# Optimization experiments

Measured on AMD Instinct MI355X. Metric: run time of the kernel, lower is better.

Reference implementation:

```python
import jax, jax.numpy as jnp
import numpy as np

N, M, C_IN, T, V = 64, 2, 3, 300, 25
C_ENC, C_DEC, K = 64, 64, 3
INTER = C_ENC // 4  # coff_embedding = 4 in 2s-AGCN unit_gcn
EPS_BN = 1e-5


def _bn(x, gamma, beta):
    # nn.BatchNorm2d in training mode: biased batch stats over (N, H, W), channel axis=1
    mean = x.mean(axis=(0, 2, 3), keepdims=True)
    var = x.var(axis=(0, 2, 3), keepdims=True)
    return gamma[None, :, None, None] * (x - mean) * jax.lax.rsqrt(var + EPS_BN) + beta[None, :, None, None]


def _unit_gcn(x, A, PA, wa, ba, wb, bb, wd, bd, gamma, beta, down_fn):
    # x: (N,C,T,V); A,PA: (K,V,V); wa/wb: (K,inter,C); wd: (K,Cout,C)  (1x1 convs)
    n, c, t, v = x.shape
    inter = wa.shape[1]
    Ahat = A + PA
    fa = jnp.einsum('nctv,kic->nkitv', x, wa) + ba[None, :, :, None, None]
    fb = jnp.einsum('nctv,kic->nkitv', x, wb) + bb[None, :, :, None, None]
    # torch: matmul((N,V,inter*T),(N,inter*T,V)) / (inter*T), softmax over dim -2 (rows)
    att = jnp.einsum('nkitv,nkitw->nkvw', fa, fb) / (inter * t)
    att = jax.nn.softmax(att, axis=-2) + Ahat[None]
    z = jnp.einsum('nctv,nkvw->nkctw', x, att)           # (N,K,C,T,V)
    y = jnp.einsum('nkctw,koc->notw', z, wd) + bd.sum(0)[None, :, None, None]
    y = _bn(y, gamma, beta)
    y = y + down_fn(x)
    return jax.nn.relu(y)


def _forward(x, A, integration_param, ram_gamma, ram_beta,
             enc_PA, enc_wa, enc_ba, enc_wb, enc_bb, enc_wd, enc_bd, enc_gamma, enc_beta,
             enc_dw, enc_db, enc_dgamma, enc_dbeta,
             dec_PA, dec_wa, dec_ba, dec_wb, dec_bb, dec_wd, dec_bd, dec_gamma, dec_beta):
    xa = x[:, 0]  # (N,C,T,V) person a
    xb = x[:, 1]  # (N,C,T,V) person b

    # --- geometric component ---
    g = jnp.einsum('nctv,nctw->nctvw', jnp.exp(xa), jnp.exp(-xb))  # (N,C,T,V,V)
    g = jnp.log(g + 1e-5) ** 2
    RAM_g = jnp.exp((-1.0 / 3.0) * g.sum(axis=1))                  # (N,T,V,V)

    # --- relative attention component ---
    enc_down = lambda h: _bn(jnp.einsum('nctv,oc->notv', h, enc_dw) + enc_db[None, :, None, None],
                             enc_dgamma, enc_dbeta)
    ident = lambda h: h  # decoder has in==out channels -> identity residual
    p1 = _unit_gcn(xa, A, enc_PA, enc_wa, enc_ba, enc_wb, enc_bb, enc_wd, enc_bd, enc_gamma, enc_beta, enc_down)
    p2 = _unit_gcn(xb, A, enc_PA, enc_wa, enc_ba, enc_wb, enc_bb, enc_wd, enc_bd, enc_gamma, enc_beta, enc_down)
    p1 = _unit_gcn(p1, A, dec_PA, dec_wa, dec_ba, dec_wb, dec_bb, dec_wd, dec_bd, dec_gamma, dec_beta, ident)
    p2 = _unit_gcn(p2, A, dec_PA, dec_wa, dec_ba, dec_wb, dec_bb, dec_wd, dec_bd, dec_gamma, dec_beta, ident)
    RAM_r = jnp.einsum('nctv,nctw->ntvw', p1, p2)                  # (N,T,V,V)
    RAM_r = _bn(RAM_r, ram_gamma, ram_beta)                        # BN over T channels
    RAM_r = (jnp.tanh(RAM_r) + 1.0) / 2.0                          # scaledTanh

    pct = (jnp.tanh(integration_param) + 1.0) / 2.0                # scalar gate
    RAM = pct * RAM_r + (1.0 - pct) * RAM_g

    # abnormal mask: variance over joints (dim=3, unbiased), summed over channels
    ab = jnp.var(xb, axis=3, ddof=1).sum(axis=1)                   # (N,T)
    ab = jnp.where(ab < 1e-4, 0.0, 1.0)
    RAM = RAM * ab[:, :, None, None]

    # normalizeRAM
    RAM = jnp.where(RAM < 0.5, 0.0, RAM)
    da = RAM.sum(axis=2)                                           # (N,T,W)
    db = RAM.sum(axis=3)                                           # (N,T,V)
    norm = jnp.einsum('ntv,ntw->ntvw', db, da)
    RAM = RAM * jax.lax.rsqrt(norm + 1e-5)
    return RAM


def setup_inputs() -> dict:
    key = jax.random.key(0)
    ks = jax.random.split(key, 12)
    f32 = jnp.float32
    rn = lambda k, s, sc=0.1: jax.random.normal(k, s, dtype=f32) * sc
    inp = {}
    inp['x'] = jax.random.normal(ks[0], (N, M, C_IN, T, V), dtype=f32)
    inp['A'] = jax.random.uniform(ks[1], (K, V, V), dtype=f32)
    inp['integration_param'] = jnp.zeros((1,), f32)
    inp['ram_gamma'] = jnp.ones((T,), f32)
    inp['ram_beta'] = jnp.zeros((T,), f32)
    inp['enc_PA'] = rn(ks[2], (K, V, V), 1e-3)
    inp['enc_wa'] = rn(ks[3], (K, INTER, C_IN)); inp['enc_ba'] = jnp.zeros((K, INTER), f32)
    inp['enc_wb'] = rn(ks[4], (K, INTER, C_IN)); inp['enc_bb'] = jnp.zeros((K, INTER), f32)
    inp['enc_wd'] = rn(ks[5], (K, C_ENC, C_IN)); inp['enc_bd'] = jnp.zeros((K, C_ENC), f32)
    inp['enc_gamma'] = jnp.ones((C_ENC,), f32); inp['enc_beta'] = jnp.zeros((C_ENC,), f32)
    inp['enc_dw'] = rn(ks[6], (C_ENC, C_IN)); inp['enc_db'] = jnp.zeros((C_ENC,), f32)
    inp['enc_dgamma'] = jnp.ones((C_ENC,), f32); inp['enc_dbeta'] = jnp.zeros((C_ENC,), f32)
    inp['dec_PA'] = rn(ks[7], (K, V, V), 1e-3)
    inp['dec_wa'] = rn(ks[8], (K, INTER, C_ENC)); inp['dec_ba'] = jnp.zeros((K, INTER), f32)
    inp['dec_wb'] = rn(ks[9], (K, INTER, C_ENC)); inp['dec_bb'] = jnp.zeros((K, INTER), f32)
    inp['dec_wd'] = rn(ks[10], (K, C_DEC, C_ENC)); inp['dec_bd'] = jnp.zeros((K, C_DEC), f32)
    inp['dec_gamma'] = jnp.ones((C_DEC,), f32); inp['dec_beta'] = jnp.zeros((C_DEC,), f32)
    return inp


def reference(x, A, integration_param, ram_gamma, ram_beta,
              enc_PA, enc_wa, enc_ba, enc_wb, enc_bb, enc_wd, enc_bd, enc_gamma, enc_beta,
              enc_dw, enc_db, enc_dgamma, enc_dbeta,
              dec_PA, dec_wa, dec_ba, dec_wb, dec_bb, dec_wd, dec_bd, dec_gamma, dec_beta):
    return _forward(x, A, integration_param, ram_gamma, ram_beta,
                    enc_PA, enc_wa, enc_ba, enc_wb, enc_bb, enc_wd, enc_bd, enc_gamma, enc_beta,
                    enc_dw, enc_db, enc_dgamma, enc_dbeta,
                    dec_PA, dec_wa, dec_ba, dec_wb, dec_bb, dec_wd, dec_bd, dec_gamma, dec_beta)
```

## Files before the change

### kernel.cpp

```cpp
#include <hip/hip_runtime.h>
#include <math.h>

#define N_     64
#define Mn     2
#define Tn     300
#define Vn     25
#define Kk     3
#define CIN    3
#define CE     64
#define INTER_ 16
#define TV     7500
#define VV     625
#define ESEG   5
#define DSEG   15
#define EYB    12

typedef float f4 __attribute__((ext_vector_type(4)));
typedef float f2 __attribute__((ext_vector_type(2)));

#define OFF_ATTP  0L
#define OFF_PART  0L
#define OFF_ATTEP 1200000L
#define OFF_ATTDP 1468800L
#define OFF_COV   1776000L
#define OFF_PCT   1780320L
#define OFF_YC    1781088L
#define OFF_TST   1781344L
#define OFF_DWDT  1781944L
#define OFF_WABT  1794232L
#define WS_REQ    1800376L

#define AEP_BR 134400
#define ADP_BR 153600

__global__ __launch_bounds__(640)
void att_kernel(const float* __restrict__ x,
                const float* __restrict__ wa, const float* __restrict__ ba,
                const float* __restrict__ wb, const float* __restrict__ bb,
                float* __restrict__ att_partial)
{
    int b = blockIdx.x;
    int s = b % ESEG;
    int k = (b / ESEG) % Kk;
    int n = (b / (ESEG * Kk)) % N_;
    int br = b / (ESEG * Kk * N_);
    const float* xp = x + (long)br * (CIN * TV) + (long)n * (Mn * CIN * TV);

    __shared__ float xs[CIN][Vn];
    __shared__ float fa_s[INTER_][Vn];
    __shared__ float fb_s[INTER_][Vn];

    int tid = threadIdx.x;
    float acc = 0.f;
    const int TSEG = Tn / ESEG;
    int t0 = s * TSEG;
    for (int t = t0; t < t0 + TSEG; ++t) {
        __syncthreads();
        for (int idx = tid; idx < CIN * Vn; idx += 640) {
            int c = idx / Vn, v = idx % Vn;
            xs[c][v] = xp[(long)c * TV + t * Vn + v];
        }
        __syncthreads();
        for (int idx = tid; idx < 2 * INTER_ * Vn; idx += 640) {
            int j = idx;
            const float* w; const float* bias; float (*dst)[Vn];
            if (j < INTER_ * Vn) { w = wa; bias = ba; dst = fa_s; }
            else { j -= INTER_ * Vn; w = wb; bias = bb; dst = fb_s; }
            int i = j / Vn, v = j % Vn;
            float sum = bias[k * INTER_ + i];
            const float* wr = w + (k * INTER_ + i) * CIN;
            #pragma unroll
            for (int c = 0; c < CIN; ++c) sum += wr[c] * xs[c][v];
            dst[i][v] = sum;
        }
        __syncthreads();
        if (tid < VV) {
            int v = tid / Vn, w = tid % Vn;
            float a = 0.f;
            #pragma unroll
            for (int i = 0; i < INTER_; ++i) a += fa_s[i][v] * fb_s[i][w];
            acc += a;
        }
    }
    if (tid < VV)
        att_partial[(((long)((br * N_ + n) * Kk + k)) * ESEG + s) * VV + tid] = acc;
}

template<int SEGS, int PADW>
__global__ __launch_bounds__(256)
void softmax_kernel(const float* __restrict__ att_partial,
                    const float* __restrict__ A, const float* __restrict__ PA,
                    float* __restrict__ attP)
{
    int b = blockIdx.x;
    int k = b % Kk;
    __shared__ float as[VV];
    int tid = threadIdx.x;
    for (int idx = tid; idx < VV; idx += 256) {
        float s = 0.f;
        for (int seg = 0; seg < SEGS; ++seg)
            s += att_partial[((long)b * SEGS + seg) * VV + idx];
        as[idx] = s * (1.0f / (INTER_ * Tn));
    }
    __syncthreads();
    if (tid < Vn) {
        int w = tid;
        float m = -1e30f;
        #pragma unroll
        for (int v = 0; v < Vn; ++v) m = fmaxf(m, as[v * Vn + w]);
        float e[Vn];
        float den = 0.f;
        #pragma unroll
        for (int v = 0; v < Vn; ++v) { e[v] = expf(as[v * Vn + w] - m); den += e[v]; }
        float inv = 1.f / den;
        #pragma unroll
        for (int v = 0; v < Vn; ++v)
            attP[((long)b * Vn + v) * PADW + w] =
                e[v] * inv + A[k * VV + v * Vn + w] + PA[k * VV + v * Vn + w];
    } else if (tid < PADW) {
        #pragma unroll
        for (int v = 0; v < Vn; ++v)
            attP[((long)b * Vn + v) * PADW + tid] = 0.f;
    }
}

__global__ __launch_bounds__(256)
void xcov_kernel(const float* __restrict__ x, double* __restrict__ part)
{
    int br = blockIdx.x / 120, g = blockIdx.x % 120;
    const float* xbase = x + (long)br * (CIN * TV);
    double a[9];
    #pragma unroll
    for (int q = 0; q < 9; ++q) a[q] = 0.0;
    for (long idx = (long)g * 256 + threadIdx.x; idx < (long)N_ * TV;
         idx += 120L * 256) {
        int n = (int)(idx / TV);
        int j = (int)(idx % TV);
        const float* xp = xbase + (long)n * (Mn * CIN * TV) + j;
        float x0 = xp[0], x1 = xp[TV], x2 = xp[2 * TV];
        a[0] += x0; a[1] += x1; a[2] += x2;
        a[3] += (double)x0 * x0; a[4] += (double)x0 * x1; a[5] += (double)x0 * x2;
        a[6] += (double)x1 * x1; a[7] += (double)x1 * x2; a[8] += (double)x2 * x2;
    }
    __shared__ double red[256];
    int tid = threadIdx.x;
    for (int q = 0; q < 9; ++q) {
        red[tid] = a[q];
        __syncthreads();
        for (int off = 128; off > 0; off >>= 1) {
            if (tid < off) red[tid] += red[tid + off];
            __syncthreads();
        }
        if (tid == 0) part[(long)blockIdx.x * 9 + q] = red[0];
        __syncthreads();
    }
}

__global__ __launch_bounds__(256)
void ey_stat_kernel(const float* __restrict__ x, const float* __restrict__ attEpB,
                    const float* __restrict__ ewd, float* __restrict__ part)
{
    __shared__ float attE_s[Kk][Vn][Vn];
    __shared__ float ewd_s[Kk * CE * CIN];
    __shared__ float xs[CIN][Vn];
    __shared__ float ez[Kk * CIN * Vn];
    __shared__ float ys[CE][Vn];
    int b = blockIdx.x, tb = b % EYB, n = (b / EYB) % N_, br = b / (EYB * N_);
    const float* attEp = attEpB + (long)br * AEP_BR;
    const float* xb = x + (long)br * (CIN * TV);
    int tid = threadIdx.x;
    for (int i = tid; i < Kk * VV; i += 256) {
        int k = i / 625, r = i - k * 625, v = r / 25, w = r - (r / 25) * 25;
        ((float*)attE_s)[i] = attEp[(long)n * 2100 + (k * 25 + v) * 28 + w];
    }
    for (int i = tid; i < Kk * CE * CIN; i += 256) ewd_s[i] = ewd[i];
    float s1 = 0.f, s2 = 0.f;
    for (int t = tb * 25; t < tb * 25 + 25; ++t) {
        const float* xp = xb + (long)n * (Mn * CIN * TV) + t * Vn;
        __syncthreads();
        for (int i = tid; i < CIN * Vn; i += 256) { int c = i / Vn, v = i % Vn; xs[c][v] = xp[c * TV + v]; }
        __syncthreads();
        for (int i = tid; i < Kk * CIN * Vn; i += 256) {
            int w = i % Vn, c = (i / Vn) % CIN, k = i / (Vn * CIN);
            float s = 0.f;
            #pragma unroll
            for (int v = 0; v < Vn; ++v) s += xs[c][v] * attE_s[k][v][w];
            ez[i] = s;
        }
        __syncthreads();
        for (int i = tid; i < CE * Vn; i += 256) {
            int w = i % Vn, o = i / Vn;
            float y = 0.f;
            #pragma unroll
            for (int k = 0; k < Kk; ++k)
                #pragma unroll
                for (int c = 0; c < CIN; ++c)
                    y += ewd_s[(k * CE + o) * CIN + c] * ez[(k * CIN + c) * Vn + w];
            ys[o][w] = y;
        }
        __syncthreads();
        if (tid < CE) {
            #pragma unroll
            for (int w = 0; w < Vn; ++w) { float y = ys[tid][w]; s1 += y; s2 += y * y; }
        }
    }
    if (tid < CE) { part[(long)b * 128 + tid * 2] = s1; part[(long)b * 128 + tid * 2 + 1] = s2; }
}

__global__ __launch_bounds__(64)
void enc_fin_kernel(const float* __restrict__ partB,
                    const double* __restrict__ covpB,
                    const float* __restrict__ eg, const float* __restrict__ ebt,
                    const float* __restrict__ edw, const float* __restrict__ edb,
                    const float* __restrict__ edg, const float* __restrict__ edbt,
                    float* __restrict__ pcTB)
{
    int br = blockIdx.x;
    const float* part = partB + (long)br * (N_ * EYB * 128);
    const double* covp = covpB + (long)br * (120 * 9);
    float* pcT = pcTB + br * 384;
    int o = threadIdx.x;
    __shared__ double tot[9];
    if (o < 9) { double s = 0; for (int g = 0; g < 120; ++g) s += covp[(long)g * 9 + o]; tot[o] = s; }
    double s1 = 0, s2 = 0;
    for (int b = 0; b < N_ * EYB; ++b) { s1 += part[(long)b * 128 + o * 2]; s2 += part[(long)b * 128 + o * 2 + 1]; }
    __syncthreads();
    double cnt = (double)N_ * Tn * Vn;
    double mean = s1 / cnt, var = s2 / cnt - mean * mean;
    double ersig = 1.0 / sqrt(var + 1e-5);
    double alpha = (double)eg[o] * ersig;
    double inv = 1.0 / cnt;
    double mu0 = tot[0] * inv, mu1 = tot[1] * inv, mu2 = tot[2] * inv;
    double c00 = tot[3] * inv - mu0 * mu0, c01 = tot[4] * inv - mu0 * mu1, c02 = tot[5] * inv - mu0 * mu2;
    double c11 = tot[6] * inv - mu1 * mu1, c12 = tot[7] * inv - mu1 * mu2, c22 = tot[8] * inv - mu2 * mu2;
    double w0 = edw[o * CIN + 0], w1 = edw[o * CIN + 1], w2 = edw[o * CIN + 2];
    double dmean = w0 * mu0 + w1 * mu1 + w2 * mu2 + (double)edb[o];
    double dvar = w0 * w0 * c00 + w1 * w1 * c11 + w2 * w2 * c22
                + 2.0 * (w0 * w1 * c01 + w0 * w2 * c02 + w1 * w2 * c12);
    double drsig = 1.0 / sqrt(dvar + 1e-5);
    double dga = (double)edg[o] * drsig;
    pcT[0 * 64 + o] = (float)alpha;
    pcT[1 * 64 + o] = (float)((double)ebt[o] - (double)eg[o] * mean * ersig
                              + dga * ((double)edb[o] - dmean) + (double)edbt[o]);
    pcT[2 * 64 + o] = (float)(dga * w0);
    pcT[3 * 64 + o] = (float)(dga * w1);
    pcT[4 * 64 + o] = (float)(dga * w2);
    pcT[5 * 64 + o] = 0.f;
}

__global__ __launch_bounds__(256)
void tr_dwd_kernel(const float* __restrict__ dwd, float* __restrict__ outp)
{
    int i = blockIdx.x * 256 + threadIdx.x;
    if (i < Kk * CE * CE) {
        int k = i / (CE * CE), r = i % (CE * CE);
        int o = r >> 6, c = r & 63;
        outp[((long)k * CE + c) * CE + o] = dwd[i];
    }
}

__global__ __launch_bounds__(256)
void tr_wab_kernel(const float* __restrict__ dwa, const float* __restrict__ dwb,
                   float* __restrict__ outp)
{
    int i = blockIdx.x * 256 + threadIdx.x;
    if (i < CE * 96) {
        int c = i / 96, j = i % 96;
        float v = (j < 48) ? dwa[j * CE + c] : dwb[(j - 48) * CE + c];
        outp[i] = v;
    }
}

__device__ __forceinline__ void penc_tile(int tid, int NT, const float* xp,
    const float (*attE_s)[Vn][Vn], const float* ewd_s, const float (*pc_s)[6],
    float (*xs)[Vn], float* ez, float (*ps)[26])
{
    __syncthreads();
    for (int i = tid; i < CIN * Vn; i += NT) { int c = i / Vn, v = i % Vn; xs[c][v] = xp[c * TV + v]; }
    __syncthreads();
    for (int i = tid; i < Kk * CIN * Vn; i += NT) {
        int w = i % Vn, c = (i / Vn) % CIN, k = i / (Vn * CIN);
        float s = 0.f;
        #pragma unroll
        for (int v = 0; v < Vn; ++v) s += xs[c][v] * attE_s[k][v][w];
        ez[i] = s;
    }
    __syncthreads();
    for (int i = tid; i < CE * Vn; i += NT) {
        int w = i % Vn, o = i / Vn;
        float y = 0.f;
        #pragma unroll
        for (int k = 0; k < Kk; ++k)
            #pragma unroll
            for (int c = 0; c < CIN; ++c)
                y += ewd_s[(k * CE + o) * CIN + c] * ez[(k * CIN + c) * Vn + w];
        float val = pc_s[o][0] * y + pc_s[o][1]
                  + pc_s[o][2] * xs[0][w] + pc_s[o][3] * xs[1][w] + pc_s[o][4] * xs[2][w];
        ps[o][w] = fmaxf(val, 0.f);
    }
    for (int i = tid; i < CE; i += NT) ps[i][25] = 0.f;
    __syncthreads();
}

__global__ __launch_bounds__(512)
void datt_kernel(const float* __restrict__ x, const float* __restrict__ attEpB,
                 const float* __restrict__ ewd, const float* __restrict__ pcTB,
                 const float* __restrict__ wabTg,
                 const float* __restrict__ dba, const float* __restrict__ dbb,
                 float* __restrict__ attp)
{
    __shared__ float attE_s[Kk][Vn][Vn];
    __shared__ float ewd_s[Kk * CE * CIN];
    __shared__ float pc_s[CE][6];
    __shared__ float bias_s[96];
    __shared__ float xs[CIN][Vn];
    __shared__ float ez[Kk * CIN * Vn];
    __shared__ __align__(16) float ps[CE][26];
    __shared__ __align__(16) float fab[96][26];
    int b = blockIdx.x, s = b % DSEG, n = (b / DSEG) % N_, br = b / (DSEG * N_);
    const float* attEp = attEpB + (long)br * AEP_BR;
    const float* pcT = pcTB + br * 384;
    const float* xb = x + (long)br * (CIN * TV);
    int tid = threadIdx.x;
    for (int i = tid; i < Kk * VV; i += 512) {
        int k = i / 625, r = i - k * 625, v = r / 25, w = r - (r / 25) * 25;
        ((float*)attE_s)[i] = attEp[(long)n * 2100 + (k * 25 + v) * 28 + w];
    }
    for (int i = tid; i < Kk * CE * CIN; i += 512) ewd_s[i] = ewd[i];
    for (int i = tid; i < CE * 6; i += 512) pc_s[i & 63][i >> 6] = pcT[i];
    for (int i = tid; i < 96; i += 512) bias_s[i] = (i < 48) ? dba[i] : dbb[i - 48];

    int sk = tid / 169, sr = tid % 169;
    int sv0 = (sr / 13) * 2, sw0 = (sr % 13) * 2;
    float acc00 = 0.f, acc01 = 0.f, acc10 = 0.f, acc11 = 0.f;
    int fj0 = (tid / 13) * 4, fv0 = (tid % 13) * 2;

    const int TS = Tn / DSEG;
    for (int t = s * TS; t < s * TS + TS; ++t) {
        const float* xp = xb + (long)n * (Mn * CIN * TV) + t * Vn;
        penc_tile(tid, 512, xp, attE_s, ewd_s, pc_s, xs, ez, ps);
        if (tid < 312) {
            float ft[4][2] = {{0.f,0.f},{0.f,0.f},{0.f,0.f},{0.f,0.f}};
            const float* wg = wabTg + fj0;
            #pragma unroll 8
            for (int c = 0; c < 64; ++c) {
                f4 wv = *(const f4*)&wg[c * 96];
                f2 pv = *(const f2*)&ps[c][fv0];
                #pragma unroll
                for (int j = 0; j < 4; ++j) {
                    ft[j][0] += wv[j] * pv[0];
                    ft[j][1] += wv[j] * pv[1];
                }
            }
            #pragma unroll
            for (int j = 0; j < 4; ++j) {
                f2 r = { ft[j][0] + bias_s[fj0 + j], ft[j][1] + bias_s[fj0 + j] };
                *(f2*)&fab[fj0 + j][fv0] = r;
            }
        }
        __syncthreads();
        if (tid < 507) {
            #pragma unroll
            for (int i = 0; i < INTER_; ++i) {
                f2 a = *(const f2*)&fab[sk * INTER_ + i][sv0];
                f2 bb2 = *(const f2*)&fab[48 + sk * INTER_ + i][sw0];
                acc00 += a[0] * bb2[0]; acc01 += a[0] * bb2[1];
                acc10 += a[1] * bb2[0]; acc11 += a[1] * bb2[1];
            }
        }
    }
    if (tid < 507) {
        long ob = (((long)((br * N_ + n) * Kk + sk)) * DSEG + s) * VV;
        attp[ob + sv0 * 25 + sw0] = acc00;
        if (sw0 + 1 < 25)                 attp[ob + sv0 * 25 + sw0 + 1] = acc01;
        if (sv0 + 1 < 25)                 attp[ob + (sv0 + 1) * 25 + sw0] = acc10;
        if (sv0 + 1 < 25 && sw0 + 1 < 25) attp[ob + (sv0 + 1) * 25 + sw0 + 1] = acc11;
    }
}

template<int TTC>
__global__ __launch_bounds__(128)
void decy0_kernel(const float* __restrict__ x,
                  const float* __restrict__ attEp,
                  const float* __restrict__ attDp,
                  const float* __restrict__ ewd,
                  const float* __restrict__ pcTg,
                  const float* __restrict__ dwdTg,
                  float* __restrict__ outp)
{
    constexpr int TBc = Tn / TTC;
    __shared__ __align__(16) float psT[25][68];
    __shared__ __align__(16) float dz_s[64][36];
    __shared__ __align__(16) float attD_s[Kk][25][32];
    __shared__ __align__(16) float ewdT_s[9][64];
    __shared__ __align__(16) float ez_s[9][28];
    __shared__ float xs[3][25];

    int b = blockIdx.x;
    int br = b / (N_ * TBc);
    int rem = b - br * (N_ * TBc);
    int n = rem / TBc, tb = rem - (rem / TBc) * TBc;
    int tid = threadIdx.x;
    int tq = tid >> 3, tw8 = tid & 7;
    int q0 = tq * 4, w0 = tw8 * 4;

    for (int i = tid; i < 576; i += 128) {
        int kc = i >> 6, o = i & 63;
        int k = kc / 3, c = kc - k * 3;
        ewdT_s[kc][o] = ewd[(k * 64 + o) * 3 + c];
    }
    for (int i = tid; i < 600; i += 128) {
        int r = i * 4;
        *(f4*)&((float*)attD_s)[r] = *(const f4*)&attDp[(long)br * ADP_BR + n * 2400 + r];
    }

    float s1_[4] = {0.f,0.f,0.f,0.f}, s2_[4] = {0.f,0.f,0.f,0.f};

    for (int tt = 0; tt < TTC; ++tt) {
        int t = tb * TTC + tt;
        __syncthreads();
        for (int i = tid; i < 75; i += 128) {
            int c = i / 25, v = i - (i / 25) * 25;
            xs[c][v] = x[(long)br * (CIN * TV) + (long)n * (Mn * CIN * TV)
                         + c * TV + t * 25 + v];
        }
        __syncthreads();
        if (tid < 72) {
            int kc = tid >> 3, wg = tid & 7;
            if (wg < 7) {
                int k = kc / 3, c = kc - k * 3;
                const float* aE = attEp + (long)br * AEP_BR + n * 2100 + k * 700;
                float e0 = 0.f, e1 = 0.f, e2 = 0.f, e3 = 0.f;
                #pragma unroll
                for (int v = 0; v < 25; ++v) {
                    f4 ae = *(const f4*)&aE[v * 28 + wg * 4];
                    float xv = xs[c][v];
                    e0 += xv * ae[0]; e1 += xv * ae[1];
                    e2 += xv * ae[2]; e3 += xv * ae[3];
                }
                f4 r = { e0, e1, e2, e3 };
                *(f4*)&ez_s[kc][wg * 4] = r;
            }
        }
        __syncthreads();
        for (int g = tid; g < 400; g += 128) {
            int og = (g & 15) << 2, w = g >> 4;
            float y0 = 0.f, y1 = 0.f, y2 = 0.f, y3 = 0.f;
            #pragma unroll
            for (int kc = 0; kc < 9; ++kc) {
                f4 wt = *(const f4*)&ewdT_s[kc][og];
                float ev = ez_s[kc][w];
                y0 += wt[0] * ev; y1 += wt[1] * ev;
                y2 += wt[2] * ev; y3 += wt[3] * ev;
            }
            const float* pcb = pcTg + br * 384;
            f4 al = *(const f4*)&pcb[0 * 64 + og];
            f4 be = *(const f4*)&pcb[1 * 64 + og];
            f4 d0 = *(const f4*)&pcb[2 * 64 + og];
            f4 d1 = *(const f4*)&pcb[3 * 64 + og];
            f4 d2 = *(const f4*)&pcb[4 * 64 + og];
            float x0 = xs[0][w], x1 = xs[1][w], x2 = xs[2][w];
            f4 r;
            r[0] = fmaxf(al[0] * y0 + be[0] + d0[0] * x0 + d1[0] * x1 + d2[0] * x2, 0.f);
            r[1] = fmaxf(al[1] * y1 + be[1] + d0[1] * x0 + d1[1] * x1 + d2[1] * x2, 0.f);
            r[2] = fmaxf(al[2] * y2 + be[2] + d0[2] * x0 + d1[2] * x1 + d2[2] * x2, 0.f);
            r[3] = fmaxf(al[3] * y3 + be[3] + d0[3] * x0 + d1[3] * x1 + d2[3] * x2, 0.f);
            *(f4*)&psT[w][og] = r;
        }
        float acc[4][4];
        #pragma unroll
        for (int j = 0; j < 4; ++j)
            #pragma unroll
            for (int m = 0; m < 4; ++m) acc[j][m] = 0.f;
        for (int k = 0; k < Kk; ++k) {
            __syncthreads();
            {
                float dzt[4][4];
                #pragma unroll
                for (int j = 0; j < 4; ++j)
                    #pragma unroll
                    for (int m = 0; m < 4; ++m) dzt[j][m] = 0.f;
                for (int v = 0; v < 25; ++v) {
                    f4 pa = *(const f4*)&psT[v][q0];
                    f4 ad = *(const f4*)&attD_s[k][v][w0];
                    #pragma unroll
                    for (int j = 0; j < 4; ++j)
                        #pragma unroll
                        for (int m = 0; m < 4; ++m) dzt[j][m] += pa[j] * ad[m];
                }
                #pragma unroll
                for (int j = 0; j < 4; ++j) {
                    f4 wv = { dzt[j][0], dzt[j][1], dzt[j][2], dzt[j][3] };
                    *(f4*)&dz_s[q0 + j][w0] = wv;
                }
            }
            __syncthreads();
            const float* wgp = dwdTg + k * 4096 + q0;
            #pragma unroll 8
            for (int c = 0; c < 64; ++c) {
                f4 wv = *(const f4*)&wgp[c * 64];
                f4 zv = *(const f4*)&dz_s[c][w0];
                #pragma unroll
                for (int j = 0; j < 4; ++j)
                    #pragma unroll
                    for (int m = 0; m < 4; ++m) acc[j][m] += wv[j] * zv[m];
            }
        }
        #pragma unroll
        for (int m = 0; m < 4; ++m) if (w0 + m < 25)
            #pragma unroll
            for (int j = 0; j < 4; ++j) {
                float a = acc[j][m]; s1_[j] += a; s2_[j] += a * a;
            }
    }
    float* red = (float*)dz_s;
    #pragma unroll
    for (int pass = 0; pass < 2; ++pass) {
        __syncthreads();
        #pragma unroll
        for (int j = 0; j < 4; ++j)
            red[(q0 + j) * 8 + tw8] = pass ? s2_[j] : s1_[j];
        __syncthreads();
        if (tid < 64) {
            float a = 0.f;
            #pragma unroll
            for (int q = 0; q < 8; ++q) a += red[tid * 8 + q];
            long pb = (((long)br * N_ + n) * TBc + tb) * 128;
            outp[pb + tid * 2 + pass] = a;
        }
    }
}

template<int TTC>
__global__ __launch_bounds__(256)
void decy1_kernel(const float* __restrict__ x,
                  const float* __restrict__ attEp,
                  const float* __restrict__ attDp,
                  const float* __restrict__ ewd,
                  const float* __restrict__ pcTg,
                  const float* __restrict__ ycb,
                  const float* __restrict__ dwdTg,
                  float* __restrict__ outp)
{
    constexpr int TBc = Tn / TTC;
    __shared__ __align__(16) float psT[2][25][68];
    __shared__ __align__(16) float dz_s[2][64][36];
    __shared__ __align__(16) float attD_s[2][Kk][25][32];
    __shared__ __align__(16) float ewdT_s[9][64];
    __shared__ __align__(16) float ez_s[2][9][28];
    __shared__ float xs[2][3][25];

    int b = blockIdx.x, tb = b % TBc, n = b / TBc;
    int tid = threadIdx.x;
    int u = tid >> 7, tl = tid & 127;
    int tq = tl >> 3, tw8 = tl & 7;
    int q0 = tq * 4, w0 = tw8 * 4;

    for (int i = tid; i < 576; i += 256) {
        int kc = i >> 6, o = i & 63;
        int k = kc / 3, c = kc - k * 3;
        ewdT_s[kc][o] = ewd[(k * 64 + o) * 3 + c];
    }
    for (int i = tid; i < 1200; i += 256) {
        int u2 = i / 600, r = (i - u2 * 600) * 4;
        *(f4*)&((float*)attD_s)[u2 * 2400 + r] =
            *(const f4*)&attDp[(long)u2 * ADP_BR + n * 2400 + r];
    }

    for (int tt = 0; tt < TTC; ++tt) {
        int t = tb * TTC + tt;
        __syncthreads();
        for (int i = tid; i < 150; i += 256) {
            int uu = i / 75, r = i - uu * 75, c = r / 25, v = r - (r / 25) * 25;
            xs[uu][c][v] = x[(((long)n * 2 + uu) * 3 + c) * TV + t * 25 + v];
        }
        __syncthreads();
        if (tid < 144) {
            int u2 = tid >= 72; int gg = tid - u2 * 72;
            int kc = gg >> 3, wg = gg & 7;
            if (wg < 7) {
                int k = kc / 3, c = kc - k * 3;
                const float* aE = attEp + u2 * AEP_BR + n * 2100 + k * 700;
                float e0 = 0.f, e1 = 0.f, e2 = 0.f, e3 = 0.f;
                #pragma unroll
                for (int v = 0; v < 25; ++v) {
                    f4 ae = *(const f4*)&aE[v * 28 + wg * 4];
                    float xv = xs[u2][c][v];
                    e0 += xv * ae[0]; e1 += xv * ae[1];
                    e2 += xv * ae[2]; e3 += xv * ae[3];
                }
                f4 r = { e0, e1, e2, e3 };
                *(f4*)&ez_s[u2][kc][wg * 4] = r;
            }
        }
        __syncthreads();
        for (int g = tid; g < 800; g += 256) {
            int u2 = g >= 400; int gg = g - u2 * 400;
            int og = (gg & 15) << 2, w = gg >> 4;
            float y0 = 0.f, y1 = 0.f, y2 = 0.f, y3 = 0.f;
            #pragma unroll
            for (int kc = 0; kc < 9; ++kc) {
                f4 wt = *(const f4*)&ewdT_s[kc][og];
                float ev = ez_s[u2][kc][w];
                y0 += wt[0] * ev; y1 += wt[1] * ev;
                y2 += wt[2] * ev; y3 += wt[3] * ev;
            }
            const float* pcb = pcTg + u2 * 384;
            f4 al = *(const f4*)&pcb[0 * 64 + og];
            f4 be = *(const f4*)&pcb[1 * 64 + og];
            f4 d0 = *(const f4*)&pcb[2 * 64 + og];
            f4 d1 = *(const f4*)&pcb[3 * 64 + og];
            f4 d2 = *(const f4*)&pcb[4 * 64 + og];
            float x0 = xs[u2][0][w], x1 = xs[u2][1][w], x2 = xs[u2][2][w];
            f4 r;
            r[0] = fmaxf(al[0] * y0 + be[0] + d0[0] * x0 + d1[0] * x1 + d2[0] * x2, 0.f);
            r[1] = fmaxf(al[1] * y1 + be[1] + d0[1] * x0 + d1[1] * x1 + d2[1] * x2, 0.f);
            r[2] = fmaxf(al[2] * y2 + be[2] + d0[2] * x0 + d1[2] * x1 + d2[2] * x2, 0.f);
            r[3] = fmaxf(al[3] * y3 + be[3] + d0[3] * x0 + d1[3] * x1 + d2[3] * x2, 0.f);
            *(f4*)&psT[u2][w][og] = r;
        }
        float acc[4][4];
        #pragma unroll
        for (int j = 0; j < 4; ++j)
            #pragma unroll
            for (int m = 0; m < 4; ++m) acc[j][m] = 0.f;
        for (int k = 0; k < Kk; ++k) {
            __syncthreads();
            {
                float dzt[4][4];
                #pragma unroll
                for (int j = 0; j < 4; ++j)
                    #pragma unroll
                    for (int m = 0; m < 4; ++m) dzt[j][m] = 0.f;
                for (int v = 0; v < 25; ++v) {
                    f4 pa = *(const f4*)&psT[u][v][q0];
                    f4 ad = *(const f4*)&attD_s[u][k][v][w0];
                    #pragma unroll
                    for (int j = 0; j < 4; ++j)
                        #pragma unroll
                        for (int m = 0; m < 4; ++m) dzt[j][m] += pa[j] * ad[m];
                }
                #pragma unroll
                for (int j = 0; j < 4; ++j) {
                    f4 wv = { dzt[j][0], dzt[j][1], dzt[j][2], dzt[j][3] };
                    *(f4*)&dz_s[u][q0 + j][w0] = wv;
                }
            }
            __syncthreads();
            const float* wgp = dwdTg + k * 4096 + q0;
            #pragma unroll 8
            for (int c = 0; c < 64; ++c) {
                f4 wv = *(const f4*)&wgp[c * 64];
                f4 zv = *(const f4*)&dz_s[u][c][w0];
                #pragma unroll
                for (int j = 0; j < 4; ++j)
                    #pragma unroll
                    for (int m = 0; m < 4; ++m) acc[j][m] += wv[j] * zv[m];
            }
        }
        {
            const float* ycu = ycb + u * 128;
            #pragma unroll
            for (int m = 0; m < 4; ++m) {
                int w = w0 + m;
                if (w < 25) {
                    #pragma unroll
                    for (int j = 0; j < 4; ++j) {
                        float pd = ycu[(q0 + j) * 2] * acc[j][m]
                                 + ycu[(q0 + j) * 2 + 1] + psT[u][w][q0 + j];
                        psT[u][w][q0 + j] = fmaxf(pd, 0.f);
                    }
                }
            }
        }
        __syncthreads();
        if (tid < 169) {
            int tv = tid / 13, tw2 = tid % 13;
            int v0 = tv * 2, ww0 = tw2 * 2;
            float r00 = 0.f, r01 = 0.f, r10 = 0.f, r11 = 0.f;
            for (int c = 0; c < 64; c += 4) {
                f4 a0 = *(const f4*)&psT[0][v0][c];
                f4 a1 = *(const f4*)&psT[0][v0 + 1][c];
                f4 b0 = *(const f4*)&psT[1][ww0][c];
                f4 b1 = *(const f4*)&psT[1][ww0 + 1][c];
                #pragma unroll
                for (int q = 0; q < 4; ++q) {
                    r00 += a0[q] * b0[q]; r01 += a0[q] * b1[q];
                    r10 += a1[q] * b0[q]; r11 += a1[q] * b1[q];
                }
            }
            long ob = ((long)n * Tn + t) * VV;
            outp[ob + v0 * 25 + ww0] = r00;
            if (ww0 + 1 < 25)                outp[ob + v0 * 25 + ww0 + 1] = r01;
            if (v0 + 1 < 25)                 outp[ob + (v0 + 1) * 25 + ww0] = r10;
            if (v0 + 1 < 25 && ww0 + 1 < 25) outp[ob + (v0 + 1) * 25 + ww0 + 1] = r11;
        }
    }
}

__global__ __launch_bounds__(64)
void dec_fin_kernel(const float* __restrict__ partB, int nparts,
                    const float* __restrict__ dg, const float* __restrict__ dbt,
                    float* __restrict__ ycB)
{
    int br = blockIdx.x;
    const float* part = partB + (long)br * nparts * 128;
    float* yc = ycB + br * 128;
    int o = threadIdx.x;
    double s1 = 0, s2 = 0;
    for (int b = 0; b < nparts; ++b) { s1 += part[(long)b * 128 + o * 2]; s2 += part[(long)b * 128 + o * 2 + 1]; }
    double cnt = (double)N_ * Tn * Vn;
    double mean = s1 / cnt, var = s2 / cnt - mean * mean;
    double rsig = 1.0 / sqrt(var + 1e-5);
    double a = (double)dg[o] * rsig;
    yc[o * 2 + 0] = (float)a;
    yc[o * 2 + 1] = (float)((double)dbt[o] - a * mean);
}

__global__ __launch_bounds__(256)
void rrbn_kernel(const float* __restrict__ rr, float* __restrict__ tstats)
{
    int t = blockIdx.x;
    double s = 0.0, s2 = 0.0;
    for (int idx = threadIdx.x; idx < N_ * VV; idx += 256) {
        int n = idx / VV, j = idx % VV;
        float v = rr[((long)n * Tn + t) * VV + j];
        s += v; s2 += (double)v * v;
    }
    __shared__ double rs[256], rs2[256];
    int tid = threadIdx.x;
    rs[tid] = s; rs2[tid] = s2;
    __syncthreads();
    for (int off = 128; off > 0; off >>= 1) {
        if (tid < off) { rs[tid] += rs[tid + off]; rs2[tid] += rs2[tid + off]; }
        __syncthreads();
    }
    if (tid == 0) {
        double cnt = (double)N_ * VV;
        double mean = rs[0] / cnt;
        double var = rs2[0] / cnt - mean * mean;
        tstats[t * 2 + 0] = (float)mean;
        tstats[t * 2 + 1] = (float)(1.0 / sqrt(var + 1e-5));
    }
}

__global__ __launch_bounds__(128)
void final_kernel(const float* __restrict__ tstats,
                  const float* __restrict__ x, const float* __restrict__ iparam,
                  const float* __restrict__ tgamma, const float* __restrict__ tbeta,
                  float* out)
{
    int b = blockIdx.x;
    int t = b % Tn, n = b / Tn;
    __shared__ float xa_s[CIN][Vn], xb_s[CIN][Vn];
    __shared__ float ram_s[VV];
    __shared__ float da_s[Vn], db_s[Vn];
    __shared__ float varc[CIN];
    __shared__ float abf;
    int tid = threadIdx.x;

    for (int idx = tid; idx < 2 * CIN * Vn; idx += 128) {
        int half = idx / (CIN * Vn);
        int r = idx % (CIN * Vn);
        int c = r / Vn, v = r % Vn;
        float val = x[(((long)n * Mn + half) * CIN + c) * TV + t * Vn + v];
        if (half == 0) xa_s[c][v] = val; else xb_s[c][v] = val;
    }
    __syncthreads();
    if (tid < CIN) {
        float s = 0.f, s2 = 0.f;
        #pragma unroll
        for (int v = 0; v < Vn; ++v) { float q = xb_s[tid][v]; s += q; s2 += q * q; }
        float mean = s / Vn;
        varc[tid] = (s2 - Vn * mean * mean) / (Vn - 1);
    }
    __syncthreads();
    if (tid == 0) {
        float absum = varc[0] + varc[1] + varc[2];
        abf = (absum < 1e-4f) ? 0.f : 1.f;
    }
    float pct = 0.5f * (tanhf(iparam[0]) + 1.f);
    float mt = tstats[t * 2], rt = tstats[t * 2 + 1];
    float gt = tgamma[t], bt = tbeta[t];
    __syncthreads();

    for (int idx = tid; idx < VV; idx += 128) {
        int v = idx / Vn, w = idx % Vn;
        float rrv = out[(long)b * VV + idx];
        float rbn = gt * (rrv - mt) * rt + bt;
        float ramr = 0.5f * (tanhf(rbn) + 1.f);
        float gsum = 0.f;
        #pragma unroll
        for (int c = 0; c < CIN; ++c) {
            float d = expf(xa_s[c][v]) * expf(-xb_s[c][w]);
            float l = logf(d + 1e-5f);
            gsum += l * l;
        }
        float ramg = expf(-(1.f / 3.f) * gsum);
        float ram = pct * ramr + (1.f - pct) * ramg;
        ram *= abf;
        if (ram < 0.5f) ram = 0.f;
        ram_s[idx] = ram;
    }
    __syncthreads();
    if (tid < Vn) {
        float s = 0.f;
        #pragma unroll
        for (int v = 0; v < Vn; ++v) s += ram_s[v * Vn + tid];
        da_s[tid] = s;
    } else if (tid >= 64 && tid < 64 + Vn) {
        int v = tid - 64;
        float s = 0.f;
        #pragma unroll
        for (int w = 0; w < Vn; ++w) s += ram_s[v * Vn + w];
        db_s[v] = s;
    }
    __syncthreads();
    for (int idx = tid; idx < VV; idx += 128) {
        int v = idx / Vn, w = idx % Vn;
        float ram = ram_s[idx];
        out[(long)b * VV + idx] = ram * rsqrtf(db_s[v] * da_s[w] + 1e-5f);
    }
}

extern "C" void kernel_launch(void* const* d_in, const int* in_sizes, int n_in,
                              void* d_out, int out_size, void* d_ws, size_t ws_size,
                              hipStream_t stream)
{
    const float* x    = (const float*)d_in[0];
    const float* A    = (const float*)d_in[1];
    const float* ip   = (const float*)d_in[2];
    const float* rg   = (const float*)d_in[3];
    const float* rbta = (const float*)d_in[4];
    const float* ePA  = (const float*)d_in[5];
    const float* ewa  = (const float*)d_in[6];
    const float* eba  = (const float*)d_in[7];
    const float* ewb  = (const float*)d_in[8];
    const float* ebb  = (const float*)d_in[9];
    const float* ewd  = (const float*)d_in[10];
    const float* ebd  = (const float*)d_in[11];  (void)ebd;
    const float* eg   = (const float*)d_in[12];
    const float* ebt  = (const float*)d_in[13];
    const float* edw  = (const float*)d_in[14];
    const float* edb  = (const float*)d_in[15];
    const float* edg  = (const float*)d_in[16];
    const float* edbt = (const float*)d_in[17];
    const float* dPA  = (const float*)d_in[18];
    const float* dwa  = (const float*)d_in[19];
    const float* dba  = (const float*)d_in[20];
    const float* dwb  = (const float*)d_in[21];
    const float* dbb  = (const float*)d_in[22];
    const float* dwd  = (const float*)d_in[23];
    const float* dbd  = (const float*)d_in[24];  (void)dbd;
    const float* dg   = (const float*)d_in[25];
    const float* dbt  = (const float*)d_in[26];

    if (ws_size < (size_t)WS_REQ * sizeof(float)) return;

    float* ws    = (float*)d_ws;
    float* attp  = ws + OFF_ATTP;
    float* part  = ws + OFF_PART;
    float* attEp = ws + OFF_ATTEP;
    float* attDp = ws + OFF_ATTDP;
    double* covp = (double*)(ws + OFF_COV);
    float* pcT   = ws + OFF_PCT;
    float* yc    = ws + OFF_YC;
    float* tst   = ws + OFF_TST;
    float* dwdTg = ws + OFF_DWDT;
    float* wabTg = ws + OFF_WABT;
    float* outf  = (float*)d_out;

    tr_dwd_kernel<<<(Kk * CE * CE + 255) / 256, 256, 0, stream>>>(dwd, dwdTg);
    tr_wab_kernel<<<(CE * 96 + 255) / 256, 256, 0, stream>>>(dwa, dwb, wabTg);

    att_kernel<<<2 * N_ * Kk * ESEG, 640, 0, stream>>>(
        x, ewa, eba, ewb, ebb, attp);
    softmax_kernel<ESEG, 28><<<2 * N_ * Kk, 256, 0, stream>>>(attp, A, ePA, attEp);
    xcov_kernel<<<240, 256, 0, stream>>>(x, covp);
    ey_stat_kernel<<<2 * N_ * EYB, 256, 0, stream>>>(x, attEp, ewd, part);
    enc_fin_kernel<<<2, 64, 0, stream>>>(part, covp, eg, ebt, edw, edb, edg, edbt, pcT);
    datt_kernel<<<2 * N_ * DSEG, 512, 0, stream>>>(
        x, attEp, ewd, pcT, wabTg, dba, dbb, outf);
    softmax_kernel<DSEG, 32><<<2 * N_ * Kk, 256, 0, stream>>>(outf, A, dPA, attDp);

    decy0_kernel<5><<<2 * N_ * (Tn / 5), 128, 0, stream>>>(
        x, attEp, attDp, ewd, pcT, dwdTg, part);
    dec_fin_kernel<<<2, 64, 0, stream>>>(part, N_ * (Tn / 5), dg, dbt, yc);
    decy1_kernel<3><<<N_ * (Tn / 3), 256, 0, stream>>>(
        x, attEp, attDp, ewd, pcT, yc, dwdTg, outf);

    rrbn_kernel<<<Tn, 256, 0, stream>>>(outf, tst);
    final_kernel<<<N_ * Tn, 128, 0, stream>>>(tst, x, ip, rg, rbta, outf);
}
```

Before: 3.899 ms.

## Re-tile decoder GCN kernel to process persons sequentially and stage params in LDS

The decy1 kernel now has all 256 threads work on one person at a time, each with a 4x2 output tile, instead of splitting the threads across the two persons with 4x4 tiles. This halves the dz_s shared buffer and lowers register pressure, at the cost of twice as many barrier-separated k-loop passes per time step. The pcT and yc parameter tables are copied into LDS once per block rather than read from global memory. Time steps per block drop from 3 to 2, which launches more blocks.

Result: slower. 4.426 ms (+13.5%).

```diff
diff --git a/kernel.cpp b/kernel.cpp
--- a/kernel.cpp
+++ b/kernel.cpp
@@ -544,17 +544,19 @@
 {
     constexpr int TBc = Tn / TTC;
     __shared__ __align__(16) float psT[2][25][68];
-    __shared__ __align__(16) float dz_s[2][64][36];
+    __shared__ __align__(16) float dz_s[64][36];
     __shared__ __align__(16) float attD_s[2][Kk][25][32];
     __shared__ __align__(16) float ewdT_s[9][64];
     __shared__ __align__(16) float ez_s[2][9][28];
+    __shared__ __align__(16) float pcT_s[2][6][64];
+    __shared__ __align__(16) float yc_s[2][64][2];
     __shared__ float xs[2][3][25];
 
     int b = blockIdx.x, tb = b % TBc, n = b / TBc;
     int tid = threadIdx.x;
-    int u = tid >> 7, tl = tid & 127;
-    int tq = tl >> 3, tw8 = tl & 7;
-    int q0 = tq * 4, w0 = tw8 * 4;
+    int tq = tid >> 4;
+    int tw16 = tid & 15;
+    int q0 = tq * 4, w0 = tw16 * 2;
 
     for (int i = tid; i < 576; i += 256) {
         int kc = i >> 6, o = i & 63;
@@ -566,6 +568,8 @@
         *(f4*)&((float*)attD_s)[u2 * 2400 + r] =
             *(const f4*)&attDp[(long)u2 * ADP_BR + n * 2400 + r];
     }
+    for (int i = tid; i < 768; i += 256) ((float*)pcT_s)[i] = pcTg[i];
+    for (int i = tid; i < 256; i += 256) ((float*)yc_s)[i] = ycb[i];
 
     for (int tt = 0; tt < TTC; ++tt) {
         int t = tb * TTC + tt;
@@ -605,7 +609,7 @@
                 y0 += wt[0] * ev; y1 += wt[1] * ev;
                 y2 += wt[2] * ev; y3 += wt[3] * ev;
             }
-            const float* pcb = pcTg + u2 * 384;
+            const float* pcb = &pcT_s[u2][0][0];
             f4 al = *(const f4*)&pcb[0 * 64 + og];
             f4 be = *(const f4*)&pcb[1 * 64 + og];
             f4 d0 = *(const f4*)&pcb[2 * 64 + og];
@@ -619,56 +623,50 @@
             r[3] = fmaxf(al[3] * y3 + be[3] + d0[3] * x0 + d1[3] * x1 + d2[3] * x2, 0.f);
             *(f4*)&psT[u2][w][og] = r;
         }
-        float acc[4][4];
-        #pragma unroll
-        for (int j = 0; j < 4; ++j)
-            #pragma unroll
-            for (int m = 0; m < 4; ++m) acc[j][m] = 0.f;
-        for (int k = 0; k < Kk; ++k) {
-            __syncthreads();
-            {
-                float dzt[4][4];
-                #pragma unroll
-                for (int j = 0; j < 4; ++j)
+        for (int u2 = 0; u2 < 2; ++u2) {
+            float acc[4][2] = {{0.f,0.f},{0.f,0.f},{0.f,0.f},{0.f,0.f}};
+            for (int k = 0; k < Kk; ++k) {
+                __syncthreads();
+                {
+                    float dzt[4][2] = {{0.f,0.f},{0.f,0.f},{0.f,0.f},{0.f,0.f}};
+                    for (int v = 0; v < 25; ++v) {
+                        f4 pa = *(const f4*)&psT[u2][v][q0];
+                        f2 ad = *(const f2*)&attD_s[u2][k][v][w0];
+                        #pragma unroll
+                        for (int j = 0; j < 4; ++j) {
+                            dzt[j][0] += pa[j] * ad[0];
+                            dzt[j][1] += pa[j] * ad[1];
+                        }
+                    }
                     #pragma unroll
-                    for (int m = 0; m < 4; ++m) dzt[j][m] = 0.f;
-                for (int v = 0; v < 25; ++v) {
-                    f4 pa = *(const f4*)&psT[u][v][q0];
-                    f4 ad = *(const f4*)&attD_s[u][k][v][w0];
+                    for (int j = 0; j < 4; ++j) {
+                        f2 wv = { dzt[j][0], dzt[j][1] };
+                        *(f2*)&dz_s[q0 + j][w0] = wv;
+                    }
+                }
+                __syncthreads();
+                const float* wgp = dwdTg + k * 4096 + q0;
+                #pragma unroll 8
+                for (int c = 0; c < 64; ++c) {
+                    f4 wv = *(const f4*)&wgp[c * 64];
+                    f2 zv = *(const f2*)&dz_s[c][w0];
                     #pragma unroll
-                    for (int j = 0; j < 4; ++j)
-                        #pragma unroll
-                        for (int m = 0; m < 4; ++m) dzt[j][m] += pa[j] * ad[m];
+                    for (int j = 0; j < 4; ++j) {
+                        acc[j][0] += wv[j] * zv[0];
+                        acc[j][1] += wv[j] * zv[1];
+                    }
                 }
-                #pragma unroll
-                for (int j = 0; j < 4; ++j) {
-                    f4 wv = { dzt[j][0], dzt[j][1], dzt[j][2], dzt[j][3] };
-                    *(f4*)&dz_s[u][q0 + j][w0] = wv;
-                }
-            }
-            __syncthreads();
-            const float* wgp = dwdTg + k * 4096 + q0;
-            #pragma unroll 8
-            for (int c = 0; c < 64; ++c) {
-                f4 wv = *(const f4*)&wgp[c * 64];
-                f4 zv = *(const f4*)&dz_s[u][c][w0];
-                #pragma unroll
-                for (int j = 0; j < 4; ++j)
-                    #pragma unroll
-                    for (int m = 0; m < 4; ++m) acc[j][m] += wv[j] * zv[m];
-            }
-        }
-        {
-            const float* ycu = ycb + u * 128;
-            #pragma unroll
-            for (int m = 0; m < 4; ++m) {
+            }
+            const float* ycu = &yc_s[u2][0][0];
+            #pragma unroll
+            for (int m = 0; m < 2; ++m) {
                 int w = w0 + m;
                 if (w < 25) {
                     #pragma unroll
                     for (int j = 0; j < 4; ++j) {
                         float pd = ycu[(q0 + j) * 2] * acc[j][m]
-                                 + ycu[(q0 + j) * 2 + 1] + psT[u][w][q0 + j];
-                        psT[u][w][q0 + j] = fmaxf(pd, 0.f);
+                                 + ycu[(q0 + j) * 2 + 1] + psT[u2][w][q0 + j];
+                        psT[u2][w][q0 + j] = fmaxf(pd, 0.f);
                     }
                 }
             }
@@ -886,7 +884,7 @@
     decy0_kernel<5><<<2 * N_ * (Tn / 5), 128, 0, stream>>>(
         x, attEp, attDp, ewd, pcT, dwdTg, part);
     dec_fin_kernel<<<2, 64, 0, stream>>>(part, N_ * (Tn / 5), dg, dbt, yc);
-    decy1_kernel<3><<<N_ * (Tn / 3), 256, 0, stream>>>(
+    decy1_kernel<2><<<N_ * (Tn / 2), 256, 0, stream>>>(
         x, attEp, attDp, ewd, pcT, yc, dwdTg, outf);
 
     rrbn_kernel<<<Tn, 256, 0, stream>>>(outf, tst);
```
